# Performance work log

Hardware: AMD Instinct MI355X
Metric: run time of the kernel (lower is better)

The kernel has to match this reference:

```python
import jax, jax.numpy as jnp
import numpy as np

DIM = 256
HEADS = 8
HEAD_DIM = DIM // HEADS
WS = 8           # window_size
TOPK = 4
BN_EPS = 1e-5


def _window_partition(x, ws):
    b, c, h, w = x.shape
    pad_h = (ws - h % ws) % ws
    pad_w = (ws - w % ws) % ws
    x = jnp.pad(x, ((0, 0), (0, 0), (0, pad_h), (0, pad_w)))
    hp, wp = x.shape[-2:]
    x = x.reshape(b, c, hp // ws, ws, wp // ws, ws)
    x = jnp.transpose(x, (0, 2, 4, 3, 5, 1)).reshape(b, -1, ws * ws, c)
    return x, (hp, wp)


def _window_reverse(windows, padded_hw, original_hw, ws):
    b, num_windows, tokens, c = windows.shape
    hp, wp = padded_hw
    x = windows.reshape(b, hp // ws, wp // ws, ws, ws, c)
    x = jnp.transpose(x, (0, 5, 1, 3, 2, 4)).reshape(b, c, hp, wp)
    h, w = original_hw
    return x[:, :, :h, :w]


def setup_inputs() -> dict:
    key = jax.random.key(0)
    ks = jax.random.split(key, 9)
    b, c, h, w = 8, DIM, 64, 64
    s = 1.0 / np.sqrt(c)
    return {
        "x": jax.random.normal(ks[0], (b, c, h, w), jnp.float32),
        "prompt": jax.random.normal(ks[1], (b, c, h, w), jnp.float32),
        "Wq": jax.random.normal(ks[2], (c, c), jnp.float32) * s,
        "Wk": jax.random.normal(ks[3], (c, c), jnp.float32) * s,
        "Wv": jax.random.normal(ks[4], (c, c), jnp.float32) * s,
        "Wproj": jax.random.normal(ks[5], (c, c), jnp.float32) * s,
        "Wg": jax.random.normal(ks[6], (c, 2 * c), jnp.float32) * (1.0 / np.sqrt(2 * c)),
        "bn_gamma": jnp.ones((c,), jnp.float32),
        "bn_beta": jnp.zeros((c,), jnp.float32),
    }


def reference(x, prompt, Wq, Wk, Wv, Wproj, Wg, bn_gamma, bn_beta):
    b, c, h, w = x.shape
    x_windows, padded_hw = _window_partition(x, WS)        # [b, nwx, T, c]
    p_windows, _ = _window_partition(prompt, WS)           # [b, nwp, T, c]
    T = WS * WS

    # --- routing: window descriptors -> topk prompt windows per query window
    x_desc = x_windows.mean(axis=2)                        # [b, nwx, c]
    p_desc = p_windows.mean(axis=2)                        # [b, nwp, c]
    score = jnp.einsum("bqc,bkc->bqk", x_desc, p_desc) / jnp.sqrt(jnp.float32(c))
    topk = min(TOPK, p_windows.shape[1])
    routed = jax.lax.top_k(score, topk)[1]                 # [b, nwx, topk]

    # --- gather routed kv windows (vmapped per-batch gather)
    selected = jax.vmap(lambda pw, idx: pw[idx])(p_windows, routed)  # [b, nwx, topk, T, c]
    nwx = x_windows.shape[1]
    kv = selected.reshape(b, nwx, topk * T, c)

    # --- windowed cross-attention (float32 internally, like the torch module)
    def heads_split(t):
        return jnp.transpose(
            t.reshape(t.shape[0], t.shape[1], t.shape[2], HEADS, HEAD_DIM),
            (0, 1, 3, 2, 4))                                # [b, nw, H, L, hd]

    q = heads_split(jnp.einsum("bnqc,oc->bnqo", x_windows, Wq).astype(jnp.float32))
    k = heads_split(jnp.einsum("bnkc,oc->bnko", kv, Wk).astype(jnp.float32))
    v = heads_split(jnp.einsum("bnkc,oc->bnko", kv, Wv).astype(jnp.float32))

    attn = jnp.einsum("bnhqd,bnhkd->bnhqk", q, k) * (HEAD_DIM ** -0.5)
    attn = jax.nn.softmax(attn, axis=-1)
    out = jnp.einsum("bnhqk,bnhkd->bnhqd", attn, v)
    out = jnp.transpose(out, (0, 1, 3, 2, 4)).reshape(b, nwx, T, c).astype(x.dtype)
    y_windows = jnp.einsum("bnqc,oc->bnqo", out, Wproj)

    y = _window_reverse(y_windows, padded_hw, (h, w), WS)  # [b, c, h, w]

    # --- gate: 1x1 conv -> BatchNorm2d (training-mode batch stats) -> sigmoid
    cat = jnp.concatenate([x, y], axis=1)                  # [b, 2c, h, w]
    g = jnp.einsum("bihw,oi->bohw", cat, Wg)
    mean = g.mean(axis=(0, 2, 3), keepdims=True)
    var = g.var(axis=(0, 2, 3), keepdims=True)             # biased, as torch BN
    g = (g - mean) * jax.lax.rsqrt(var + BN_EPS)
    g = g * bn_gamma[None, :, None, None] + bn_beta[None, :, None, None]
    gate = jax.nn.sigmoid(g)

    return x + gate * y
```

## Files before the change

kernel.cpp:

```cpp
#include <hip/hip_runtime.h>
#include <math.h>

#define B 8
#define Cc 256
#define P 4096
#define NW 64
#define NH 8
#define HD 32
#define TOPK 4
#define SCALE 0.17677669529663687f

typedef unsigned short u16;
typedef __attribute__((ext_vector_type(4))) float f32x4;
typedef __attribute__((ext_vector_type(8))) short s16x8;
typedef __attribute__((ext_vector_type(4))) unsigned short u16x4;

#define MFMA(a, b, c) __builtin_amdgcn_mfma_f32_16x16x32_bf16(a, b, c, 0, 0, 0)

__device__ inline u16 f2bf(float f) {
  unsigned u = __float_as_uint(f);
  return (u16)((u + 0x7fffu + ((u >> 16) & 1u)) >> 16);
}
__device__ inline float bf2f(u16 h) { return __uint_as_float(((unsigned)h) << 16); }

__global__ __launch_bounds__(256) void wcvt_kernel(
    const float* __restrict__ Wq, const float* __restrict__ Wk,
    const float* __restrict__ Wv, const float* __restrict__ Wproj,
    const float* __restrict__ Wg, u16* __restrict__ Wbf) {
  int job = blockIdx.y;
  const float* src;
  u16* dst;
  int n;
  switch (job) {
    case 0: src = Wq;    dst = Wbf;          n = 65536;  break;
    case 1: src = Wk;    dst = Wbf + 65536;  n = 65536;  break;
    case 2: src = Wv;    dst = Wbf + 131072; n = 65536;  break;
    case 3: src = Wproj; dst = Wbf + 196608; n = 65536;  break;
    default: src = Wg;   dst = Wbf + 262144; n = 131072; break;
  }
  int i = (blockIdx.x * 256 + threadIdx.x) * 4;
  if (i < n) {
    float4 v = *(const float4*)(src + i);
    u16x4 o = {f2bf(v.x), f2bf(v.y), f2bf(v.z), f2bf(v.w)};
    *(u16x4*)(dst + i) = o;
  }
}

__global__ __launch_bounds__(256) void pack_kernel(
    const float* __restrict__ x, const float* __restrict__ prompt,
    u16* __restrict__ XY, u16* __restrict__ PT, float* __restrict__ Pd) {
  __shared__ u16 ldsd[64 * 68];
  __shared__ float pdl[64 * 9];
  int y = blockIdx.x;
  int sb = blockIdx.y;
  int cq = blockIdx.z;
  int sel = sb >> 3, b = sb & 7;
  const float* src =
      (sel ? prompt : x) + (size_t)(b * 256 + cq * 64) * 4096 + y * 64;
  int tid = threadIdx.x;
  int pxg = tid & 15;
  int cr = tid >> 4;
  int px0 = pxg * 4;
#pragma unroll
  for (int iter = 0; iter < 4; ++iter) {
    int cl = iter * 16 + cr;
    float4 v = *(const float4*)(src + (size_t)cl * 4096 + px0);
    u16x4 o = {f2bf(v.x), f2bf(v.y), f2bf(v.z), f2bf(v.w)};
    int sw = ((cl >> 3) & 3) << 2;
    *(u16x4*)(ldsd + cl * 68 + (px0 ^ sw)) = o;
    float s4 = (v.x + v.y) + (v.z + v.w);
    float s8 = s4 + __shfl_xor(s4, 1);
    if ((pxg & 1) == 0) pdl[cl * 9 + (pxg >> 1)] = s8;
  }
  __syncthreads();
  int tok = tid >> 2, cg = tid & 3;
  int n = ((y >> 3) << 3) + (tok >> 3);
  int tk = ((y & 7) << 3) + (tok & 7);
  size_t prow = (size_t)b * 4096 + n * 64 + tk;
  u16* dst = (sel ? (PT + prow * 256) : (XY + prow * 512)) + cq * 64;
#pragma unroll
  for (int cc = 0; cc < 2; ++cc) {
    int cb = cg * 8 + cc * 32;
    s16x8 v;
#pragma unroll
    for (int j = 0; j < 8; ++j) {
      int cl = cb + j;
      int sw = ((cl >> 3) & 3) << 2;
      v[j] = (short)ldsd[cl * 68 + (tok ^ sw)];
    }
    *(s16x8*)(dst + cb) = v;
  }
  float* pd = Pd + ((size_t)sb * 64 + y) * 2048 + cq * 64;
#pragma unroll
  for (int i = 0; i < 2; ++i) {
    int e = i * 256 + tid;
    int wx = e >> 6, cl = e & 63;
    pd[wx * 256 + cl] = pdl[cl * 9 + wx];
  }
}

__global__ __launch_bounds__(256) void dred_kernel(
    const float* __restrict__ Pd, float* __restrict__ dx, float* __restrict__ dp) {
  int sb = blockIdx.x;
  int sel = sb >> 3, b = sb & 7;
  int c = threadIdx.x;
  float* dst = (sel ? dp : dx) + ((size_t)b * 256 + c) * 64;
  const float* src = Pd + (size_t)sb * 64 * 2048;
#pragma unroll
  for (int nn = 0; nn < 8; ++nn) {
    int n = blockIdx.y * 8 + nn;
    int wy = n >> 3, wx = n & 7;
    float s = 0.f;
#pragma unroll
    for (int yl = 0; yl < 8; ++yl)
      s += src[((wy * 8 + yl) * 8 + wx) * 256 + c];
    dst[n] = s * (1.f / 64.f);
  }
}

__global__ __launch_bounds__(64) void route_kernel(
    const float* __restrict__ dx, const float* __restrict__ dp,
    int* __restrict__ routed) {
  int bq = blockIdx.x;
  int b = bq >> 6;
  int q = bq & 63;
  int lane = threadIdx.x;
  const float* dxb = dx + (size_t)b * Cc * NW;
  const float* dpb = dp + (size_t)b * Cc * NW;
  float s = 0.f;
  for (int c = 0; c < Cc; ++c)
    s = fmaf(dxb[c * NW + q], dpb[c * NW + lane], s);
  s *= (1.f / 16.f);
  for (int kk = 0; kk < TOPK; ++kk) {
    float v = s;
    int i = lane;
    for (int off = 32; off; off >>= 1) {
      float ov = __shfl_xor(v, off);
      int oi = __shfl_xor(i, off);
      if (ov > v || (ov == v && oi < i)) { v = ov; i = oi; }
    }
    if (lane == 0) routed[bq * TOPK + kk] = i;
    if (lane == i) s = -INFINITY;
  }
}

__device__ __forceinline__ void gemm_core(
    const u16* __restrict__ A, int lda, const u16* __restrict__ W, int K,
    int m0, int n0, int tid, u16* Asm, u16* Wsm, f32x4 (&acc)[4][4]) {
  int l = tid & 63, wv = tid >> 6;
  int lq = l & 15, g = l >> 4;
  int wm = (wv & 1) * 64, wn = (wv >> 1) * 64;
  for (int k0 = 0; k0 < K; k0 += 64) {
    s16x8 av[4], wvv[4];
#pragma unroll
    for (int i = 0; i < 4; ++i) {
      int s = i * 256 + tid, row = s >> 3, u = s & 7;
      av[i] = *(const s16x8*)(A + (size_t)(m0 + row) * lda + k0 + u * 8);
      wvv[i] = *(const s16x8*)(W + (size_t)(n0 + row) * K + k0 + u * 8);
    }
    __syncthreads();
#pragma unroll
    for (int i = 0; i < 4; ++i) {
      int s = i * 256 + tid, row = s >> 3, u = s & 7;
      int gu = u ^ (row & 7);
      *(s16x8*)(Asm + row * 64 + gu * 8) = av[i];
      *(s16x8*)(Wsm + row * 64 + gu * 8) = wvv[i];
    }
    __syncthreads();
#pragma unroll
    for (int ks = 0; ks < 2; ++ks) {
      s16x8 af[4], bfr[4];
#pragma unroll
      for (int mi = 0; mi < 4; ++mi) {
        int r = wm + 16 * mi + lq;
        af[mi] = *(const s16x8*)(Asm + r * 64 + ((4 * ks + g) ^ (r & 7)) * 8);
      }
#pragma unroll
      for (int ni = 0; ni < 4; ++ni) {
        int r = wn + 16 * ni + lq;
        bfr[ni] = *(const s16x8*)(Wsm + r * 64 + ((4 * ks + g) ^ (r & 7)) * 8);
      }
#pragma unroll
      for (int mi = 0; mi < 4; ++mi)
#pragma unroll
        for (int ni = 0; ni < 4; ++ni)
          acc[mi][ni] = MFMA(af[mi], bfr[ni], acc[mi][ni]);
    }
  }
}

__device__ __forceinline__ void store_rowmajor(
    f32x4 (&acc)[4][4], u16* __restrict__ Out, int ldo,
    size_t mbase, int nbase, int lq, int g) {
#pragma unroll
  for (int mi = 0; mi < 4; ++mi) {
    size_t mrow = mbase + 16 * mi + 4 * g;
#pragma unroll
    for (int r = 0; r < 4; ++r) {
      u16* orow = Out + (mrow + r) * ldo + nbase + lq;
#pragma unroll
      for (int ni = 0; ni < 4; ++ni)
        orow[16 * ni] = f2bf(acc[mi][ni][r]);
    }
  }
}

__device__ __forceinline__ void store_chanmajor(
    f32x4 (&acc)[4][4], u16* __restrict__ Out,
    int bb, int tb, int cbase, int lq) {
#pragma unroll
  for (int ni = 0; ni < 4; ++ni) {
    u16* ocol = Out + ((size_t)(bb * 256) + cbase + 16 * ni + lq) * 4096 + tb;
#pragma unroll
    for (int mi = 0; mi < 4; ++mi) {
      u16x4 pk = {f2bf(acc[mi][ni][0]), f2bf(acc[mi][ni][1]),
                  f2bf(acc[mi][ni][2]), f2bf(acc[mi][ni][3])};
      *(u16x4*)(ocol + 16 * mi) = pk;
    }
  }
}

__global__ __launch_bounds__(256) void qkv_kernel(
    const u16* __restrict__ XY, const u16* __restrict__ PT,
    const u16* __restrict__ Wbf, u16* __restrict__ QT,
    u16* __restrict__ KT, u16* __restrict__ VT) {
  __shared__ u16 Asm[8192], Wsm[8192];
  int jy = blockIdx.y, m0 = blockIdx.x * 128;
  int tid = threadIdx.x;
  int l = tid & 63, wv = tid >> 6;
  int lq = l & 15, g = l >> 4;
  int wm = (wv & 1) * 64, wn = (wv >> 1) * 64;
  f32x4 acc[4][4];
#pragma unroll
  for (int mi = 0; mi < 4; ++mi)
#pragma unroll
    for (int ni = 0; ni < 4; ++ni)
      acc[mi][ni] = (f32x4){0.f, 0.f, 0.f, 0.f};

  const u16* A;
  const u16* W;
  int lda, n0;
  if (jy < 2) { A = XY; lda = 512; W = Wbf; n0 = jy * 128; }
  else        { A = PT; lda = 256; W = Wbf + 65536; n0 = (jy - 2) * 128; }
  gemm_core(A, lda, W, 256, m0, n0, tid, Asm, Wsm, acc);

  if (jy < 2) {
    store_rowmajor(acc, QT, 256, (size_t)(m0 + wm), n0 + wn, lq, g);
  } else if (n0 < 256) {
    store_rowmajor(acc, KT, 256, (size_t)(m0 + wm), n0 + wn, lq, g);
  } else {
    store_chanmajor(acc, VT, m0 >> 12, (m0 & 4095) + wm + 4 * g,
                    (n0 - 256) + wn, lq);
  }
}

__global__ __launch_bounds__(256) void proj_kernel(
    const u16* __restrict__ OT, const u16* __restrict__ Wbf,
    u16* __restrict__ XY) {
  __shared__ u16 Asm[8192], Wsm[8192];
  int m0 = blockIdx.x * 128, n0 = blockIdx.y * 128;
  int tid = threadIdx.x;
  int l = tid & 63, wv = tid >> 6;
  int lq = l & 15, g = l >> 4;
  int wm = (wv & 1) * 64, wn = (wv >> 1) * 64;
  f32x4 acc[4][4];
#pragma unroll
  for (int mi = 0; mi < 4; ++mi)
#pragma unroll
    for (int ni = 0; ni < 4; ++ni)
      acc[mi][ni] = (f32x4){0.f, 0.f, 0.f, 0.f};
  gemm_core(OT, 256, Wbf + 196608, 256, m0, n0, tid, Asm, Wsm, acc);
  store_rowmajor(acc, XY + 256, 512, (size_t)(m0 + wm), n0 + wn, lq, g);
}

__global__ __launch_bounds__(256) void gate_kernel(
    const u16* __restrict__ XY, const u16* __restrict__ Wbf,
    u16* __restrict__ GT, float* __restrict__ pS, float* __restrict__ pSS) {
  __shared__ u16 Asm[8192], Wsm[8192];
  int m0 = blockIdx.x * 128, n0 = blockIdx.y * 128;
  int tid = threadIdx.x;
  int l = tid & 63, wv = tid >> 6;
  int lq = l & 15, g = l >> 4;
  int wm = (wv & 1) * 64, wn = (wv >> 1) * 64;
  f32x4 acc[4][4];
#pragma unroll
  for (int mi = 0; mi < 4; ++mi)
#pragma unroll
    for (int ni = 0; ni < 4; ++ni)
      acc[mi][ni] = (f32x4){0.f, 0.f, 0.f, 0.f};
  gemm_core(XY, 512, Wbf + 262144, 512, m0, n0, tid, Asm, Wsm, acc);
  store_rowmajor(acc, GT, 256, (size_t)(m0 + wm), n0 + wn, lq, g);

  float cs[4], cq[4];
#pragma unroll
  for (int ni = 0; ni < 4; ++ni) {
    float s = 0.f, q2 = 0.f;
#pragma unroll
    for (int mi = 0; mi < 4; ++mi)
#pragma unroll
      for (int r = 0; r < 4; ++r) {
        float v = acc[mi][ni][r];
        s += v;
        q2 = fmaf(v, v, q2);
      }
    cs[ni] = s;
    cq[ni] = q2;
  }
#pragma unroll
  for (int ni = 0; ni < 4; ++ni) {
    cs[ni] += __shfl_xor(cs[ni], 16);
    cs[ni] += __shfl_xor(cs[ni], 32);
    cq[ni] += __shfl_xor(cq[ni], 16);
    cq[ni] += __shfl_xor(cq[ni], 32);
  }
  float* sS = (float*)Asm;
  float* sQ = sS + 128;
  __syncthreads();
  if ((wv & 1) == 0 && g == 0) {
#pragma unroll
    for (int ni = 0; ni < 4; ++ni) {
      int col = wn + 16 * ni + lq;
      sS[col] = cs[ni];
      sQ[col] = cq[ni];
    }
  }
  __syncthreads();
  if ((wv & 1) == 1 && g == 0) {
#pragma unroll
    for (int ni = 0; ni < 4; ++ni) {
      int col = wn + 16 * ni + lq;
      sS[col] += cs[ni];
      sQ[col] += cq[ni];
    }
  }
  __syncthreads();
  if (tid < 128) {
    pS[(size_t)blockIdx.x * 256 + n0 + tid] = sS[tid];
    pSS[(size_t)blockIdx.x * 256 + n0 + tid] = sQ[tid];
  }
}

__global__ __launch_bounds__(512) void attn_kernel(
    const u16* __restrict__ Qb, const u16* __restrict__ Kb,
    const u16* __restrict__ Vt, const int* __restrict__ routed,
    u16* __restrict__ Ob) {
  __shared__ u16 Plds[8 * 4096];
  int bn = blockIdx.x, b = bn >> 6, n = bn & 63;
  int h = threadIdx.x >> 6, l = threadIdx.x & 63;
  int lq = l & 15, g = l >> 4;
  char* Pw = (char*)(Plds + h * 4096);

  const u16* Qrow = Qb + ((size_t)(b * 4096) + n * 64) * 256 + h * 32 + g * 8;
  s16x8 qf[4];
#pragma unroll
  for (int qi = 0; qi < 4; ++qi)
    qf[qi] = *(const s16x8*)(Qrow + (16 * qi + lq) * 256);

  f32x4 acc[4][2];
#pragma unroll
  for (int qi = 0; qi < 4; ++qi) {
    acc[qi][0] = (f32x4){0.f, 0.f, 0.f, 0.f};
    acc[qi][1] = (f32x4){0.f, 0.f, 0.f, 0.f};
  }
  float denom[4] = {0.f, 0.f, 0.f, 0.f};
  const f32x4 zero4 = {0.f, 0.f, 0.f, 0.f};
  const int* rptr = routed + bn * TOPK;

  for (int kk = 0; kk < TOPK; ++kk) {
    int pw = __builtin_amdgcn_readfirstlane(rptr[kk]);
    const u16* Krow = Kb + ((size_t)(b * 4096) + pw * 64) * 256 + h * 32 + g * 8;
    const u16* Vrow = Vt + ((size_t)(b * 256) + h * 32 + lq) * 4096 + pw * 64 + 8 * g;
#pragma unroll
    for (int kvi = 0; kvi < 4; ++kvi) {
      s16x8 kf = *(const s16x8*)(Krow + (16 * kvi + lq) * 256);
      f32x4 sv[4];
#pragma unroll
      for (int qi = 0; qi < 4; ++qi)
        sv[qi] = MFMA(kf, qf[qi], zero4);
#pragma unroll
      for (int qi = 0; qi < 4; ++qi) {
        float p0 = __expf(sv[qi][0] * SCALE);
        float p1 = __expf(sv[qi][1] * SCALE);
        float p2 = __expf(sv[qi][2] * SCALE);
        float p3 = __expf(sv[qi][3] * SCALE);
        denom[qi] += (p0 + p1) + (p2 + p3);
        uint2 pk;
        pk.x = (unsigned)f2bf(p0) | ((unsigned)f2bf(p1) << 16);
        pk.y = (unsigned)f2bf(p2) | ((unsigned)f2bf(p3) << 16);
        int q = 16 * qi + lq;
        int kvb = (16 * kvi + 4 * g) * 2;
        *(uint2*)(Pw + q * 128 + (kvb ^ ((q & 7) << 4))) = pk;
      }
    }
#pragma unroll
    for (int s = 0; s < 2; ++s) {
      s16x8 vf[2];
#pragma unroll
      for (int di = 0; di < 2; ++di)
        vf[di] = *(const s16x8*)(Vrow + (size_t)(16 * di) * 4096 + 32 * s);
#pragma unroll
      for (int qi = 0; qi < 4; ++qi) {
        int q = 16 * qi + lq;
        s16x8 pf = *(const s16x8*)(Pw + q * 128 +
                                   ((64 * s + 16 * g) ^ ((q & 7) << 4)));
#pragma unroll
        for (int di = 0; di < 2; ++di)
          acc[qi][di] = MFMA(pf, vf[di], acc[qi][di]);
      }
    }
  }

#pragma unroll
  for (int qi = 0; qi < 4; ++qi) {
    denom[qi] += __shfl_xor(denom[qi], 16);
    denom[qi] += __shfl_xor(denom[qi], 32);
  }
  u16* Orow = Ob + ((size_t)(b * 4096) + n * 64) * 256 + h * 32;
#pragma unroll
  for (int qi = 0; qi < 4; ++qi) {
    float inv = 1.f / denom[qi];
#pragma unroll
    for (int r = 0; r < 4; ++r) {
      float nr = __shfl(inv, 4 * g + r);
#pragma unroll
      for (int di = 0; di < 2; ++di)
        Orow[(16 * qi + 4 * g + r) * 256 + 16 * di + lq] =
            f2bf(acc[qi][di][r] * nr);
    }
  }
}

__global__ __launch_bounds__(1024) void bnfin_kernel(
    const float* __restrict__ pS, const float* __restrict__ pSS,
    const float* __restrict__ gamma, const float* __restrict__ beta,
    float* __restrict__ scale, float* __restrict__ shift) {
  int tid = threadIdx.x;
  int c = tid >> 2, part = tid & 3;
  float S = 0.f, SS = 0.f;
  for (int m = part * 64; m < part * 64 + 64; ++m) {
    S += pS[m * 256 + c];
    SS += pSS[m * 256 + c];
  }
  __shared__ float rS[4][256], rQ[4][256];
  rS[part][c] = S;
  rQ[part][c] = SS;
  __syncthreads();
  if (tid < 256) {
    int cc = tid;
    float S2 = rS[0][cc] + rS[1][cc] + rS[2][cc] + rS[3][cc];
    float Q2 = rQ[0][cc] + rQ[1][cc] + rQ[2][cc] + rQ[3][cc];
    const float invN = 1.f / 32768.f;
    float mean = S2 * invN;
    float var = Q2 * invN - mean * mean;
    float sc = rsqrtf(var + 1e-5f) * gamma[cc];
    scale[cc] = sc;
    shift[cc] = beta[cc] - mean * sc;
  }
}

__global__ __launch_bounds__(256) void final_kernel(
    const float* __restrict__ x, const u16* __restrict__ XY,
    const u16* __restrict__ GT, const float* __restrict__ scale,
    const float* __restrict__ shift, float* __restrict__ out) {
  __shared__ u16 Yl[64 * 256];
  __shared__ u16 Gl[64 * 256];
  __shared__ float sSc[256], sSh[256];
  int y = blockIdx.x, b = blockIdx.y;
  int tid = threadIdx.x;
  sSc[tid] = scale[tid];
  sSh[tid] = shift[tid];
  {
    int r = tid >> 2;
    int n = ((y >> 3) << 3) + (r >> 3);
    int t = ((y & 7) << 3) + (r & 7);
    size_t prow = (size_t)b * 4096 + n * 64 + t;
    const u16* ysrc = XY + prow * 512 + 256;
    const u16* gsrc = GT + prow * 256;
#pragma unroll
    for (int cc = 0; cc < 8; ++cc) {
      int chunk = (tid & 3) * 8 + cc;
      int off = r * 256 + ((chunk ^ (r & 31)) << 3);
      *(s16x8*)(Yl + off) = *(const s16x8*)(ysrc + chunk * 8);
      *(s16x8*)(Gl + off) = *(const s16x8*)(gsrc + chunk * 8);
    }
  }
  __syncthreads();
  int lane = tid & 63, wq = tid >> 6;
  size_t base = (size_t)(b * 256) * 4096 + y * 64 + lane;
#pragma unroll 2
  for (int ch = 0; ch < 8; ++ch) {
    int chunk = wq * 8 + ch;
    int off = lane * 256 + ((chunk ^ (lane & 31)) << 3);
    s16x8 yv = *(const s16x8*)(Yl + off);
    s16x8 gv = *(const s16x8*)(Gl + off);
#pragma unroll
    for (int j = 0; j < 8; ++j) {
      int c = chunk * 8 + j;
      size_t a = base + (size_t)c * 4096;
      float gate = 1.f / (1.f + __expf(-fmaf(bf2f((u16)gv[j]), sSc[c], sSh[c])));
      out[a] = x[a] + gate * bf2f((u16)yv[j]);
    }
  }
}

extern "C" void kernel_launch(void* const* d_in, const int* in_sizes, int n_in,
                              void* d_out, int out_size, void* d_ws, size_t ws_size,
                              hipStream_t stream) {
  const float* x      = (const float*)d_in[0];
  const float* prompt = (const float*)d_in[1];
  const float* Wq     = (const float*)d_in[2];
  const float* Wk     = (const float*)d_in[3];
  const float* Wv     = (const float*)d_in[4];
  const float* Wproj  = (const float*)d_in[5];
  const float* Wg     = (const float*)d_in[6];
  const float* gamma  = (const float*)d_in[7];
  const float* beta   = (const float*)d_in[8];

  char* wsb = (char*)d_ws;
  u16* XY    = (u16*)(wsb + 0);
  u16* PT    = (u16*)(wsb + 33554432);
  u16* QT    = (u16*)(wsb + 50331648);
  u16* KT    = (u16*)(wsb + 67108864);
  u16* VT    = (u16*)(wsb + 83886080);
  u16* OT    = (u16*)(wsb + 100663296);
  u16* Wbf   = (u16*)(wsb + 117440512);
  float* dx  = (float*)(wsb + 118226944);
  float* dp  = (float*)(wsb + 118751232);
  float* scl = (float*)(wsb + 119275520);
  float* shf = (float*)(wsb + 119276544);
  int* routed = (int*)(wsb + 119277568);
  float* Pd  = (float*)QT;
  float* pS  = (float*)KT;
  float* pSS = (float*)(wsb + 67108864 + 262144);
  u16* GT = QT;

  wcvt_kernel<<<dim3(128, 5), 256, 0, stream>>>(Wq, Wk, Wv, Wproj, Wg, Wbf);
  pack_kernel<<<dim3(64, 16, 4), 256, 0, stream>>>(x, prompt, XY, PT, Pd);
  dred_kernel<<<dim3(16, 8), 256, 0, stream>>>(Pd, dx, dp);
  route_kernel<<<B * NW, 64, 0, stream>>>(dx, dp, routed);
  qkv_kernel<<<dim3(256, 6), 256, 0, stream>>>(XY, PT, Wbf, QT, KT, VT);
  attn_kernel<<<B * NW, 512, 0, stream>>>(QT, KT, VT, routed, OT);
  proj_kernel<<<dim3(256, 2), 256, 0, stream>>>(OT, Wbf, XY);
  gate_kernel<<<dim3(256, 2), 256, 0, stream>>>(XY, Wbf, GT, pS, pSS);
  bnfin_kernel<<<1, 1024, 0, stream>>>(pS, pSS, gamma, beta, scl, shf);
  final_kernel<<<dim3(64, 8), 256, 0, stream>>>(x, XY, GT, scl, shf, (float*)d_out);
}
```

Measured before the change: 165.9 us.

## Fuse output projection into attention kernel and weight conversion into pack

The attention kernel now stages its normalized per-window output tile (64 tokens x 256 channels) in swizzled LDS, then runs the Wproj GEMM in-kernel with MFMA. Each head-wave computes 32 output channels and writes y directly into the XY buffer, which removes the separate proj kernel and the OT round trip through global memory. Weight bf16 conversion is folded into pack_kernel as an extra z-slice, saving a launch. In exchange, each attention block reloads Wproj fragments from global/L2 with no LDS reuse across blocks and adds two block-wide barriers.

After: 164.2 us. Within noise of the previous version (-1.0%).

```diff
diff --git a/kernel.cpp b/kernel.cpp
--- a/kernel.cpp
+++ b/kernel.cpp
@@ -23,32 +23,35 @@
 }
 __device__ inline float bf2f(u16 h) { return __uint_as_float(((unsigned)h) << 16); }
 
-__global__ __launch_bounds__(256) void wcvt_kernel(
+__global__ __launch_bounds__(256) void pack_kernel(
+    const float* __restrict__ x, const float* __restrict__ prompt,
     const float* __restrict__ Wq, const float* __restrict__ Wk,
     const float* __restrict__ Wv, const float* __restrict__ Wproj,
-    const float* __restrict__ Wg, u16* __restrict__ Wbf) {
-  int job = blockIdx.y;
-  const float* src;
-  u16* dst;
-  int n;
-  switch (job) {
-    case 0: src = Wq;    dst = Wbf;          n = 65536;  break;
-    case 1: src = Wk;    dst = Wbf + 65536;  n = 65536;  break;
-    case 2: src = Wv;    dst = Wbf + 131072; n = 65536;  break;
-    case 3: src = Wproj; dst = Wbf + 196608; n = 65536;  break;
-    default: src = Wg;   dst = Wbf + 262144; n = 131072; break;
-  }
-  int i = (blockIdx.x * 256 + threadIdx.x) * 4;
-  if (i < n) {
-    float4 v = *(const float4*)(src + i);
-    u16x4 o = {f2bf(v.x), f2bf(v.y), f2bf(v.z), f2bf(v.w)};
-    *(u16x4*)(dst + i) = o;
-  }
-}
-
-__global__ __launch_bounds__(256) void pack_kernel(
-    const float* __restrict__ x, const float* __restrict__ prompt,
-    u16* __restrict__ XY, u16* __restrict__ PT, float* __restrict__ Pd) {
+    const float* __restrict__ Wg,
+    u16* __restrict__ XY, u16* __restrict__ PT, float* __restrict__ Pd,
+    u16* __restrict__ Wbf) {
+  if (blockIdx.z == 4) {
+    int id = blockIdx.y * 64 + blockIdx.x;
+    if (id >= 640) return;
+    int job = id >> 7;
+    const float* src;
+    u16* dst;
+    int n;
+    switch (job) {
+      case 0: src = Wq;    dst = Wbf;          n = 65536;  break;
+      case 1: src = Wk;    dst = Wbf + 65536;  n = 65536;  break;
+      case 2: src = Wv;    dst = Wbf + 131072; n = 65536;  break;
+      case 3: src = Wproj; dst = Wbf + 196608; n = 65536;  break;
+      default: src = Wg;   dst = Wbf + 262144; n = 131072; break;
+    }
+    int i = ((id & 127) * 256 + threadIdx.x) * 4;
+    if (i < n) {
+      float4 v = *(const float4*)(src + i);
+      u16x4 o = {f2bf(v.x), f2bf(v.y), f2bf(v.z), f2bf(v.w)};
+      *(u16x4*)(dst + i) = o;
+    }
+    return;
+  }
   __shared__ u16 ldsd[64 * 68];
   __shared__ float pdl[64 * 9];
   int y = blockIdx.x;
@@ -254,25 +257,6 @@
   }
 }
 
-__global__ __launch_bounds__(256) void proj_kernel(
-    const u16* __restrict__ OT, const u16* __restrict__ Wbf,
-    u16* __restrict__ XY) {
-  __shared__ u16 Asm[8192], Wsm[8192];
-  int m0 = blockIdx.x * 128, n0 = blockIdx.y * 128;
-  int tid = threadIdx.x;
-  int l = tid & 63, wv = tid >> 6;
-  int lq = l & 15, g = l >> 4;
-  int wm = (wv & 1) * 64, wn = (wv >> 1) * 64;
-  f32x4 acc[4][4];
-#pragma unroll
-  for (int mi = 0; mi < 4; ++mi)
-#pragma unroll
-    for (int ni = 0; ni < 4; ++ni)
-      acc[mi][ni] = (f32x4){0.f, 0.f, 0.f, 0.f};
-  gemm_core(OT, 256, Wbf + 196608, 256, m0, n0, tid, Asm, Wsm, acc);
-  store_rowmajor(acc, XY + 256, 512, (size_t)(m0 + wm), n0 + wn, lq, g);
-}
-
 __global__ __launch_bounds__(256) void gate_kernel(
     const u16* __restrict__ XY, const u16* __restrict__ Wbf,
     u16* __restrict__ GT, float* __restrict__ pS, float* __restrict__ pSS) {
@@ -343,7 +327,7 @@
 __global__ __launch_bounds__(512) void attn_kernel(
     const u16* __restrict__ Qb, const u16* __restrict__ Kb,
     const u16* __restrict__ Vt, const int* __restrict__ routed,
-    u16* __restrict__ Ob) {
+    const u16* __restrict__ Wp, u16* __restrict__ XY) {
   __shared__ u16 Plds[8 * 4096];
   int bn = blockIdx.x, b = bn >> 6, n = bn & 63;
   int h = threadIdx.x >> 6, l = threadIdx.x & 63;
@@ -415,19 +399,63 @@
     denom[qi] += __shfl_xor(denom[qi], 16);
     denom[qi] += __shfl_xor(denom[qi], 32);
   }
-  u16* Orow = Ob + ((size_t)(b * 4096) + n * 64) * 256 + h * 32;
+
+  __syncthreads();
+  char* Ot = (char*)Plds;
 #pragma unroll
   for (int qi = 0; qi < 4; ++qi) {
     float inv = 1.f / denom[qi];
 #pragma unroll
     for (int r = 0; r < 4; ++r) {
       float nr = __shfl(inv, 4 * g + r);
-#pragma unroll
-      for (int di = 0; di < 2; ++di)
-        Orow[(16 * qi + 4 * g + r) * 256 + 16 * di + lq] =
+      int t = 16 * qi + 4 * g + r;
+      char* rowp = Ot + t * 512;
+#pragma unroll
+      for (int di = 0; di < 2; ++di) {
+        int c = h * 32 + 16 * di + lq;
+        *(u16*)(rowp + ((c * 2) ^ ((t & 7) << 4))) =
             f2bf(acc[qi][di][r] * nr);
-    }
-  }
+      }
+    }
+  }
+  __syncthreads();
+
+  f32x4 acc2[4][2];
+#pragma unroll
+  for (int mi = 0; mi < 4; ++mi) {
+    acc2[mi][0] = (f32x4){0.f, 0.f, 0.f, 0.f};
+    acc2[mi][1] = (f32x4){0.f, 0.f, 0.f, 0.f};
+  }
+#pragma unroll
+  for (int k0 = 0; k0 < 256; k0 += 32) {
+    s16x8 af[4], bfr[2];
+#pragma unroll
+    for (int mi = 0; mi < 4; ++mi) {
+      int t = 16 * mi + lq;
+      af[mi] = *(const s16x8*)(Ot + t * 512 +
+                               (((k0 + 8 * g) * 2) ^ ((t & 7) << 4)));
+    }
+#pragma unroll
+    for (int ni = 0; ni < 2; ++ni)
+      bfr[ni] = *(const s16x8*)(Wp + (size_t)(h * 32 + 16 * ni + lq) * 256 +
+                                k0 + 8 * g);
+#pragma unroll
+    for (int mi = 0; mi < 4; ++mi)
+#pragma unroll
+      for (int ni = 0; ni < 2; ++ni)
+        acc2[mi][ni] = MFMA(af[mi], bfr[ni], acc2[mi][ni]);
+  }
+
+  u16* Yrow = XY + ((size_t)(b * 4096) + n * 64) * 512 + 256 + h * 32;
+#pragma unroll
+  for (int mi = 0; mi < 4; ++mi)
+#pragma unroll
+    for (int r = 0; r < 4; ++r) {
+      u16* orow = Yrow + (size_t)(16 * mi + 4 * g + r) * 512 + lq;
+#pragma unroll
+      for (int ni = 0; ni < 2; ++ni)
+        orow[16 * ni] = f2bf(acc2[mi][ni][r]);
+    }
 }
 
 __global__ __launch_bounds__(1024) void bnfin_kernel(
@@ -522,7 +550,6 @@
   u16* QT    = (u16*)(wsb + 50331648);
   u16* KT    = (u16*)(wsb + 67108864);
   u16* VT    = (u16*)(wsb + 83886080);
-  u16* OT    = (u16*)(wsb + 100663296);
   u16* Wbf   = (u16*)(wsb + 117440512);
   float* dx  = (float*)(wsb + 118226944);
   float* dp  = (float*)(wsb + 118751232);
@@ -534,13 +561,13 @@
   float* pSS = (float*)(wsb + 67108864 + 262144);
   u16* GT = QT;
 
-  wcvt_kernel<<<dim3(128, 5), 256, 0, stream>>>(Wq, Wk, Wv, Wproj, Wg, Wbf);
-  pack_kernel<<<dim3(64, 16, 4), 256, 0, stream>>>(x, prompt, XY, PT, Pd);
+  pack_kernel<<<dim3(64, 16, 5), 256, 0, stream>>>(
+      x, prompt, Wq, Wk, Wv, Wproj, Wg, XY, PT, Pd, Wbf);
   dred_kernel<<<dim3(16, 8), 256, 0, stream>>>(Pd, dx, dp);
   route_kernel<<<B * NW, 64, 0, stream>>>(dx, dp, routed);
   qkv_kernel<<<dim3(256, 6), 256, 0, stream>>>(XY, PT, Wbf, QT, KT, VT);
-  attn_kernel<<<B * NW, 512, 0, stream>>>(QT, KT, VT, routed, OT);
-  proj_kernel<<<dim3(256, 2), 256, 0, stream>>>(OT, Wbf, XY);
+  attn_kernel<<<B * NW, 512, 0, stream>>>(QT, KT, VT, routed,
+                                          Wbf + 196608, XY);
   gate_kernel<<<dim3(256, 2), 256, 0, stream>>>(XY, Wbf, GT, pS, pSS);
   bnfin_kernel<<<1, 1024, 0, stream>>>(pS, pSS, gamma, beta, scl, shf);
   final_kernel<<<dim3(64, 8), 256, 0, stream>>>(x, XY, GT, scl, shf, (float*)d_out);
```
